# Optimization experiments

Hardware: AMD Instinct MI355X
Metric: run time of the kernel (lower is better)

## Reference

```python
import jax, jax.numpy as jnp
import numpy as np

B, S, D = 1, 4096, 2048
H, KV, HD = 16, 4, 128
ROPE_BASE = 10000.0


def setup_inputs() -> dict:
    key = jax.random.key(0)
    ks = jax.random.split(key, 5)
    hidden_states = jax.random.normal(ks[0], (B, S, D), dtype=jnp.float32) * 0.02
    Wq = jax.random.normal(ks[1], (D, H * HD), dtype=jnp.float32) * (D ** -0.5)
    Wk = jax.random.normal(ks[2], (D, KV * HD), dtype=jnp.float32) * (D ** -0.5)
    Wv = jax.random.normal(ks[3], (D, KV * HD), dtype=jnp.float32) * (D ** -0.5)
    Wo = jax.random.normal(ks[4], (H * HD, D), dtype=jnp.float32) * ((H * HD) ** -0.5)
    # causal additive mask [1,1,S,S]
    neg = jnp.float32(-1e9)
    causal = jnp.tril(jnp.ones((S, S), dtype=bool))
    attention_mask = jnp.where(causal, 0.0, neg)[None, None, :, :].astype(jnp.float32)
    position_ids = jnp.arange(S, dtype=jnp.int32)[None, :]
    return {"hidden_states": hidden_states, "Wq": Wq, "Wk": Wk, "Wv": Wv,
            "Wo": Wo, "attention_mask": attention_mask, "position_ids": position_ids}


def _rotate_half(x):
    x1, x2 = jnp.split(x, 2, axis=-1)
    return jnp.concatenate([-x2, x1], axis=-1)


def _rope_cos_sin(position_ids):
    # position_ids: [B, S] -> cos/sin [B, 1, S, HD]
    inv_freq = 1.0 / (ROPE_BASE ** (jnp.arange(0, HD, 2, dtype=jnp.float32) / HD))
    freqs = position_ids.astype(jnp.float32)[..., None] * inv_freq  # [B,S,HD/2]
    emb = jnp.concatenate([freqs, freqs], axis=-1)                   # [B,S,HD]
    return jnp.cos(emb)[:, None, :, :], jnp.sin(emb)[:, None, :, :]


def reference(hidden_states, Wq, Wk, Wv, Wo, attention_mask, position_ids):
    bsz, q_len, _ = hidden_states.shape
    # QKV projections -> [B, heads, S, HD]
    q = (hidden_states @ Wq).reshape(bsz, q_len, H, HD).transpose(0, 2, 1, 3)
    k = (hidden_states @ Wk).reshape(bsz, q_len, KV, HD).transpose(0, 2, 1, 3)
    v = (hidden_states @ Wv).reshape(bsz, q_len, KV, HD).transpose(0, 2, 1, 3)
    # inline RoPE
    cos, sin = _rope_cos_sin(position_ids)
    q = q * cos + _rotate_half(q) * sin
    k = k * cos + _rotate_half(k) * sin
    # GQA repeat_interleave on head dim
    rep = H // KV
    k = jnp.repeat(k, rep, axis=1)
    v = jnp.repeat(v, rep, axis=1)
    # attention
    scale = HD ** -0.5
    scores = jnp.einsum('bhqd,bhkd->bhqk', q, k) * scale + attention_mask
    probs = jax.nn.softmax(scores, axis=-1)
    out = jnp.einsum('bhqk,bhkd->bhqd', probs, v)
    out = out.transpose(0, 2, 1, 3).reshape(bsz, q_len, H * HD)
    return out @ Wo
```

## Files before the change

### kernel.cpp

```cpp
#include <hip/hip_runtime.h>
#include <hip/hip_bf16.h>
#include <cstdint>
#include <cmath>

#define S_LEN 4096
#define DMODEL 2048
#define NH 16
#define NKV 4
#define HD 128
#define NQKV 3072

typedef unsigned short u16;
typedef unsigned int u32;
typedef __attribute__((ext_vector_type(8))) __bf16 bf16x8;
typedef __attribute__((ext_vector_type(4))) float f32x4;
typedef __attribute__((ext_vector_type(16))) float f32x16;
typedef __attribute__((ext_vector_type(4))) int i32x4;

__device__ __forceinline__ u16 f2bf(float f) {
  __bf16 h = (__bf16)f;
  return __builtin_bit_cast(u16, h);
}
__device__ __forceinline__ float bf2f(u16 u) {
  return (float)__builtin_bit_cast(__bf16, u);
}
__device__ __forceinline__ u32 pk2(float a, float b) {
  return (u32)f2bf(a) | ((u32)f2bf(b) << 16);
}

__device__ __forceinline__ void gload16(const void* g, void* l) {
  __builtin_amdgcn_global_load_lds(
      (const __attribute__((address_space(1))) void*)g,
      (__attribute__((address_space(3))) void*)l, 16, 0, 0);
}

__global__ void k_f32_to_bf16(const float* __restrict__ src, u16* __restrict__ dst, int n4) {
  int i = blockIdx.x * blockDim.x + threadIdx.x;
  if (i < n4) {
    float4 v = reinterpret_cast<const float4*>(src)[i];
    ushort4 o = make_ushort4(f2bf(v.x), f2bf(v.y), f2bf(v.z), f2bf(v.w));
    reinterpret_cast<ushort4*>(dst)[i] = o;
  }
}

__global__ void k_transpose_f32_bf16(const float* __restrict__ src, int srcStride,
                                     u16* __restrict__ dst, int dstStride) {
  __shared__ float tile[32][33];
  int n0 = blockIdx.x * 32, k0 = blockIdx.y * 32;
  int tx = threadIdx.x, ty = threadIdx.y;
#pragma unroll
  for (int r = 0; r < 32; r += 8)
    tile[ty + r][tx] = src[(size_t)(k0 + ty + r) * srcStride + n0 + tx];
  __syncthreads();
#pragma unroll
  for (int r = 0; r < 32; r += 8)
    dst[(size_t)(n0 + ty + r) * dstStride + k0 + tx] = f2bf(tile[tx][ty + r]);
}

__global__ void k_transpose_bf16(const u16* __restrict__ src, int srcStride,
                                 u16* __restrict__ dst, int dstStride) {
  __shared__ u16 tile[32][33];
  int n0 = blockIdx.x * 32, k0 = blockIdx.y * 32;
  int tx = threadIdx.x, ty = threadIdx.y;
#pragma unroll
  for (int r = 0; r < 32; r += 8)
    tile[ty + r][tx] = src[(size_t)(k0 + ty + r) * srcStride + n0 + tx];
  __syncthreads();
#pragma unroll
  for (int r = 0; r < 32; r += 8)
    dst[(size_t)(n0 + ty + r) * dstStride + k0 + tx] = tile[tx][ty + r];
}

__global__ void k_rope_tab(const int* __restrict__ pos_ids, float2* __restrict__ tab) {
  int idx = blockIdx.x * blockDim.x + threadIdx.x;
  int s = idx >> 6, dh = idx & 63;
  const float L2B = 13.287712379549449f;
  float pos = (float)pos_ids[s];
  float invf = exp2f(-(float)dh * (L2B / 64.0f));
  float ang = pos * invf;
  tab[idx] = make_float2(cosf(ang), sinf(ang));
}

__global__ void k_rope(const u16* __restrict__ qkv, const float2* __restrict__ tab,
                       u16* __restrict__ Qb, u16* __restrict__ Kb) {
  int s = blockIdx.x;
  const u16* row = qkv + (size_t)s * NQKV;
  const float QSCALE = 0.08838834764831845f * 1.4426950408889634f;
  for (int c = threadIdx.x; c < DMODEL + NKV * HD; c += blockDim.x) {
    int d = c & 127;
    int dh = d & 63;
    float2 cs = tab[s * 64 + dh];
    float x = bf2f(row[c]);
    float xp = bf2f(row[c ^ 64]);
    float rot = (d < 64) ? -xp : xp;
    float out = x * cs.x + rot * cs.y;
    if (c < DMODEL) {
      int h = c >> 7;
      out *= QSCALE;
      Qb[((size_t)h * S_LEN + s) * HD + d] = f2bf(out);
    } else {
      int kvh = (c - DMODEL) >> 7;
      Kb[((size_t)kvh * S_LEN + s) * HD + d] = f2bf(out);
    }
  }
}

template <int OUT_BF16>
__global__ __launch_bounds__(256) void k_gemm_bt(const u16* __restrict__ A,
                                                 const u16* __restrict__ BT,
                                                 void* __restrict__ C, int M, int N, int K) {
  __shared__ __align__(16) u16 As[128 * 32];
  __shared__ __align__(16) u16 Bs[128 * 32];
  const int tid = threadIdx.x, wave = tid >> 6, lane = tid & 63;
  const int fr = lane & 15, fq = lane >> 4;
  const int rowBase = blockIdx.y * 128, colBase = blockIdx.x * 128;
  const int wr = wave >> 1, wc = wave & 1;
  f32x4 acc[4][4] = {};
  const int nk = K >> 5;
  for (int kt = 0; kt < nk; ++kt) {
    const int k0 = kt << 5;
#pragma unroll
    for (int p = 0; p < 2; ++p) {
      int cbase = p * 256 + wave * 64;
      int chunk = cbase + lane;
      int r = chunk >> 2, cb = chunk & 3;
      gload16(A + (size_t)(rowBase + r) * K + k0 + cb * 8, (char*)As + cbase * 16);
      gload16(BT + (size_t)(colBase + r) * K + k0 + cb * 8, (char*)Bs + cbase * 16);
    }
    __syncthreads();
    bf16x8 a[4], b[4];
#pragma unroll
    for (int m = 0; m < 4; ++m)
      a[m] = *reinterpret_cast<const bf16x8*>(&As[(wr * 64 + m * 16 + fr) * 32 + fq * 8]);
#pragma unroll
    for (int n = 0; n < 4; ++n)
      b[n] = *reinterpret_cast<const bf16x8*>(&Bs[(wc * 64 + n * 16 + fr) * 32 + fq * 8]);
#pragma unroll
    for (int m = 0; m < 4; ++m)
#pragma unroll
      for (int n = 0; n < 4; ++n)
        acc[m][n] = __builtin_amdgcn_mfma_f32_16x16x32_bf16(a[m], b[n], acc[m][n], 0, 0, 0);
    __syncthreads();
  }
#pragma unroll
  for (int m = 0; m < 4; ++m) {
    int row0 = rowBase + wr * 64 + m * 16 + fq * 4;
#pragma unroll
    for (int n = 0; n < 4; ++n) {
      int col = colBase + wc * 64 + n * 16 + fr;
#pragma unroll
      for (int j = 0; j < 4; ++j) {
        if (OUT_BF16)
          ((u16*)C)[(size_t)(row0 + j) * N + col] = f2bf(acc[m][n][j]);
        else
          ((float*)C)[(size_t)(row0 + j) * N + col] = acc[m][n][j];
      }
    }
  }
}

#define OP_ESTRIDE ((size_t)NH * 32 * 128 * 128)

__device__ __forceinline__ void stage_kv64(const u16* __restrict__ Kbk,
                                           const u16* __restrict__ VTk, int kb,
                                           char* KsB, char* VsB, int tid) {
#pragma unroll
  for (int it = 0; it < 2; ++it) {
    int slot = it * 512 + tid;
    int r = slot >> 4, cb = slot & 15;
    gload16(Kbk + (size_t)(kb + r) * HD + (size_t)((cb ^ (r & 15)) * 8), KsB + slot * 16);
    int vb = slot >> 7, d = slot & 127;
    gload16(VTk + (size_t)d * S_LEN + kb + vb * 8, VsB + slot * 16);
  }
}

__device__ __forceinline__ void sl_w(float* p, int off, const f32x16& v) {
#pragma unroll
  for (int r = 0; r < 16; r += 4)
    *reinterpret_cast<float4*>(p + off + r) = make_float4(v[r], v[r + 1], v[r + 2], v[r + 3]);
}

__global__ __launch_bounds__(512, 2) void k_attn(const u16* __restrict__ Qb,
                                                 const u16* __restrict__ Kb,
                                                 const u16* __restrict__ VT,
                                                 u16* __restrict__ Op,
                                                 float2* __restrict__ mlG) {
  __shared__ __align__(16) u16 Ks[2][64 * 128];
  __shared__ __align__(16) u16 Vs[2][8 * 128 * 8];
  const int h = blockIdx.x;
  const int p = blockIdx.y;
  const int e = blockIdx.z;
  const int kv = h >> 2;
  const int tid = threadIdx.x, wave = tid >> 6, lane = tid & 63;
  const int grp = wave >> 2, pr = wave & 3;
  const int ql = lane & 31, hi = lane >> 5;
  const float DEFER_THR = 11.541560327111707f;

  const u16* Kbk = Kb + (size_t)kv * S_LEN * HD;
  const u16* VTk = VT + (size_t)kv * HD * S_LEN;

#pragma unroll 1
  for (int half = 0; half < 2; ++half) {
    const int qt = half ? p : (31 - p);
    const int qg0w = qt * 128 + pr * 32;
    const int qglob = qg0w + ql;

    __syncthreads();
    stage_kv64(Kbk, VTk, e * 64, (char*)Ks[0], (char*)Vs[0], tid);

    bf16x8 qf[8];
    {
      const u16* qp = Qb + ((size_t)h * S_LEN + qglob) * HD;
#pragma unroll
      for (int t = 0; t < 8; ++t)
        qf[t] = *reinterpret_cast<const bf16x8*>(qp + t * 16 + hi * 8);
    }
    f32x16 o[4] = {};
    float m = -INFINITY, l = 0.f;

    __syncthreads();

    int buf = 0;
    const int nkt = 2 * qt + 2;
    for (int kt = e; kt < nkt; kt += 2) {
      if (kt + 2 < nkt)
        stage_kv64(Kbk, VTk, (kt + 2) * 64, (char*)Ks[buf ^ 1], (char*)Vs[buf ^ 1], tid);
      const int kbg = kt * 64 + grp * 32;
      if (kbg <= qg0w + 31) {
        const char* Kc = (const char*)Ks[buf];
        const char* Vc = (const char*)Vs[buf];

        f32x16 st = {};
        const int r0 = grp * 32 + ql;
#pragma unroll
        for (int t = 0; t < 8; ++t) {
          int ch = (2 * t + hi) ^ (ql & 15);
          bf16x8 kf = *reinterpret_cast<const bf16x8*>(Kc + r0 * 256 + ch * 16);
          st = __builtin_amdgcn_mfma_f32_32x32x16_bf16(kf, qf[t], st, 0, 0, 0);
        }
        if (kbg + 31 > qg0w) {
#pragma unroll
          for (int r = 0; r < 16; ++r) {
            int kl = (r & 3) + 8 * (r >> 2) + 4 * hi;
            if (kbg + kl > qglob) st[r] = -1e30f;
          }
        }
        float mx[16];
#pragma unroll
        for (int r = 0; r < 16; ++r) mx[r] = st[r];
#pragma unroll
        for (int s = 8; s > 0; s >>= 1)
#pragma unroll
          for (int r = 0; r < 16; ++r)
            if (r < s) mx[r] = fmaxf(mx[r], mx[r + s]);
        float tmax = fmaxf(mx[0], __shfl_xor(mx[0], 32));
        if (__any(tmax - m > DEFER_THR)) {
          float mn = fmaxf(m, tmax);
          float corr = exp2f(m - mn);
          m = mn;
          l *= corr;
#pragma unroll
          for (int d0 = 0; d0 < 4; ++d0) o[d0] *= corr;
        }
        float sm[16];
#pragma unroll
        for (int r = 0; r < 16; ++r) {
          st[r] = exp2f(st[r] - m);
          sm[r] = st[r];
        }
#pragma unroll
        for (int s = 8; s > 0; s >>= 1)
#pragma unroll
          for (int r = 0; r < 16; ++r)
            if (r < s) sm[r] += sm[r + s];
        l += sm[0] + __shfl_xor(sm[0], 32);

        bf16x8 pa0, pa1;
        {
          u32 w0 = pk2(st[0], st[1]), w1 = pk2(st[2], st[3]);
          u32 w2 = pk2(st[4], st[5]), w3 = pk2(st[6], st[7]);
          u32 xw0 = (u32)__shfl_xor((int)w0, 32), xw1 = (u32)__shfl_xor((int)w1, 32);
          u32 xw2 = (u32)__shfl_xor((int)w2, 32), xw3 = (u32)__shfl_xor((int)w3, 32);
          i32x4 pw;
          pw[0] = (int)(hi ? xw2 : w0);
          pw[1] = (int)(hi ? xw3 : w1);
          pw[2] = (int)(hi ? w2 : xw0);
          pw[3] = (int)(hi ? w3 : xw1);
          pa0 = __builtin_bit_cast(bf16x8, pw);
          w0 = pk2(st[8], st[9]);   w1 = pk2(st[10], st[11]);
          w2 = pk2(st[12], st[13]); w3 = pk2(st[14], st[15]);
          xw0 = (u32)__shfl_xor((int)w0, 32); xw1 = (u32)__shfl_xor((int)w1, 32);
          xw2 = (u32)__shfl_xor((int)w2, 32); xw3 = (u32)__shfl_xor((int)w3, 32);
          pw[0] = (int)(hi ? xw2 : w0);
          pw[1] = (int)(hi ? xw3 : w1);
          pw[2] = (int)(hi ? w2 : xw0);
          pw[3] = (int)(hi ? w3 : xw1);
          pa1 = __builtin_bit_cast(bf16x8, pw);
        }
#pragma unroll
        for (int d0 = 0; d0 < 4; ++d0) {
          int dr = d0 * 32 + ql;
          bf16x8 vf0 = *reinterpret_cast<const bf16x8*>(
              Vc + (((grp * 4 + 0 + hi) * 128) + dr) * 16);
          o[d0] = __builtin_amdgcn_mfma_f32_32x32x16_bf16(vf0, pa0, o[d0], 0, 0, 0);
          bf16x8 vf1 = *reinterpret_cast<const bf16x8*>(
              Vc + (((grp * 4 + 2 + hi) * 128) + dr) * 16);
          o[d0] = __builtin_amdgcn_mfma_f32_32x32x16_bf16(vf1, pa1, o[d0], 0, 0, 0);
        }
      }
      __syncthreads();
      buf ^= 1;
    }

    float2* mlb = (float2*)Ks;
    if (hi == 0) mlb[(grp * 4 + pr) * 32 + ql] = make_float2(m, l);
    __syncthreads();
    float2 pml = mlb[((1 - grp) * 4 + pr) * 32 + ql];
    float mm = fmaxf(m, pml.x);
    float fa = (mm > -INFINITY) ? exp2f(m - mm) : 0.f;
    float fb = (mm > -INFINITY) ? exp2f(pml.x - mm) : 0.f;
    float ll = l * fa + pml.y * fb;
    __syncthreads();
    float* exK = (float*)Ks;
    float* exV = (float*)Vs;
    const int off = (pr * 64 + lane) * 16;
    if (grp == 0) {
      sl_w(exK, off, o[2]);
      sl_w(exK + 4096, off, o[3]);
    } else {
      sl_w(exV, off, o[0]);
      sl_w(exV + 4096, off, o[1]);
    }
    if (grp == 0 && hi == 0)
      mlG[(((size_t)e * NH + h) * 32 + qt) * 128 + pr * 32 + ql] = make_float2(mm, ll);
    __syncthreads();
    {
      u16* opRow = Op + (size_t)e * OP_ESTRIDE +
                   (((size_t)h * 32 + qt) * 128 + pr * 32 + ql) * 128;
      if (grp == 0) {
#pragma unroll
        for (int rp = 0; rp < 8; ++rp) {
          int r = 2 * rp;
          int dbase = (r & 3) + 8 * (r >> 2) + 4 * hi;
          float q0a = exV[off + r], q0b = exV[off + r + 1];
          float q1a = exV[4096 + off + r], q1b = exV[4096 + off + r + 1];
          *reinterpret_cast<u32*>(opRow + 0 * 32 + dbase) =
              pk2(o[0][r] * fa + q0a * fb, o[0][r + 1] * fa + q0b * fb);
          *reinterpret_cast<u32*>(opRow + 1 * 32 + dbase) =
              pk2(o[1][r] * fa + q1a * fb, o[1][r + 1] * fa + q1b * fb);
        }
      } else {
#pragma unroll
        for (int rp = 0; rp < 8; ++rp) {
          int r = 2 * rp;
          int dbase = (r & 3) + 8 * (r >> 2) + 4 * hi;
          float q2a = exK[off + r], q2b = exK[off + r + 1];
          float q3a = exK[4096 + off + r], q3b = exK[4096 + off + r + 1];
          *reinterpret_cast<u32*>(opRow + 2 * 32 + dbase) =
              pk2(o[2][r] * fa + q2a * fb, o[2][r + 1] * fa + q2b * fb);
          *reinterpret_cast<u32*>(opRow + 3 * 32 + dbase) =
              pk2(o[3][r] * fa + q3a * fb, o[3][r + 1] * fa + q3b * fb);
        }
      }
    }
  }
}

__global__ void k_comb(const u16* __restrict__ Op, const float2* __restrict__ mlG,
                       u16* __restrict__ AO) {
  int s = blockIdx.x, h = blockIdx.y;
  int qt = s >> 7, row = s & 127;
  int t = threadIdx.x;
  size_t base = (((size_t)h * 32 + qt) * 128 + row) * 128;
  float2 ml0 = mlG[(((size_t)0 * NH + h) * 32 + qt) * 128 + row];
  float2 ml1 = mlG[(((size_t)1 * NH + h) * 32 + qt) * 128 + row];
  float M = fmaxf(ml0.x, ml1.x);
  float w0 = (ml0.x > -INFINITY) ? exp2f(ml0.x - M) : 0.f;
  float w1 = (ml1.x > -INFINITY) ? exp2f(ml1.x - M) : 0.f;
  float inv = 1.0f / (ml0.y * w0 + ml1.y * w1);
  u32 a = *reinterpret_cast<const u32*>(Op + base + t * 2);
  u32 b = *reinterpret_cast<const u32*>(Op + OP_ESTRIDE + base + t * 2);
  float o0 = bf2f((u16)a) * w0 + bf2f((u16)b) * w1;
  float o1 = bf2f((u16)(a >> 16)) * w0 + bf2f((u16)(b >> 16)) * w1;
  *reinterpret_cast<u32*>(AO + (size_t)s * DMODEL + h * HD + t * 2) = pk2(o0 * inv, o1 * inv);
}

extern "C" void kernel_launch(void* const* d_in, const int* in_sizes, int n_in,
                              void* d_out, int out_size, void* d_ws, size_t ws_size,
                              hipStream_t stream) {
  const float* hidden = (const float*)d_in[0];
  const float* Wq = (const float*)d_in[1];
  const float* Wk = (const float*)d_in[2];
  const float* Wv = (const float*)d_in[3];
  const float* Wo = (const float*)d_in[4];
  const int* pos_ids = (const int*)d_in[6];
  float* out = (float*)d_out;

  char* ws = (char*)d_ws;
  u16* WoT  = (u16*)(ws);
  u16* Wt   = (u16*)(ws + (8ull << 20));
  u16* Qb   = (u16*)(ws + (8ull << 20));
  u16* Kb   = (u16*)(ws + (24ull << 20));
  u16* VT   = (u16*)(ws + (28ull << 20));
  u16* Xb   = (u16*)(ws + (32ull << 20));
  u16* AO   = (u16*)(ws + (32ull << 20));
  float2* tab = (float2*)(ws + (48ull << 20));
  u16* QKVb = (u16*)(ws + (50ull << 20));
  u16* Op   = (u16*)(ws + (48ull << 20));
  float2* mlG = (float2*)(ws + (80ull << 20));

  dim3 tb(32, 8);
  k_f32_to_bf16<<<dim3((S_LEN * DMODEL / 4) / 256), dim3(256), 0, stream>>>(
      hidden, Xb, S_LEN * DMODEL / 4);
  k_transpose_f32_bf16<<<dim3(64, 64), tb, 0, stream>>>(Wq, 2048, Wt, 2048);
  k_transpose_f32_bf16<<<dim3(16, 64), tb, 0, stream>>>(Wk, 512, Wt + (size_t)2048 * 2048, 2048);
  k_transpose_f32_bf16<<<dim3(16, 64), tb, 0, stream>>>(Wv, 512, Wt + (size_t)2560 * 2048, 2048);
  k_transpose_f32_bf16<<<dim3(64, 64), tb, 0, stream>>>(Wo, 2048, WoT, 2048);
  k_rope_tab<<<dim3(S_LEN * 64 / 256), dim3(256), 0, stream>>>(pos_ids, tab);

  k_gemm_bt<1><<<dim3(24, 32), 256, 0, stream>>>(Xb, Wt, QKVb, S_LEN, NQKV, DMODEL);

  k_rope<<<dim3(S_LEN), 256, 0, stream>>>(QKVb, tab, Qb, Kb);
  k_transpose_bf16<<<dim3(16, 128), tb, 0, stream>>>(QKVb + 2560, NQKV, VT, S_LEN);

  k_attn<<<dim3(NH, 16, 2), 512, 0, stream>>>(Qb, Kb, VT, Op, mlG);
  k_comb<<<dim3(S_LEN, NH), 64, 0, stream>>>(Op, mlG, AO);

  k_gemm_bt<0><<<dim3(16, 32), 256, 0, stream>>>(AO, WoT, out, S_LEN, DMODEL, DMODEL);
}
```

Before: 337.7 us.

## Restructure attention into 256-thread blocks per query tile and vectorize RoPE

```diff
diff --git a/kernel.cpp b/kernel.cpp
--- a/kernel.cpp
+++ b/kernel.cpp
@@ -86,22 +86,39 @@
   int s = blockIdx.x;
   const u16* row = qkv + (size_t)s * NQKV;
   const float QSCALE = 0.08838834764831845f * 1.4426950408889634f;
-  for (int c = threadIdx.x; c < DMODEL + NKV * HD; c += blockDim.x) {
+  const int NV = (DMODEL + NKV * HD) / 8;
+  for (int v8 = threadIdx.x; v8 < NV; v8 += blockDim.x) {
+    int c = v8 * 8;
     int d = c & 127;
-    int dh = d & 63;
-    float2 cs = tab[s * 64 + dh];
-    float x = bf2f(row[c]);
-    float xp = bf2f(row[c ^ 64]);
-    float rot = (d < 64) ? -xp : xp;
-    float out = x * cs.x + rot * cs.y;
-    if (c < DMODEL) {
+    int dh0 = d & 63;
+    bool lowh = (d < 64);
+    ushort4 a0 = *reinterpret_cast<const ushort4*>(row + c);
+    ushort4 a1 = *reinterpret_cast<const ushort4*>(row + c + 4);
+    ushort4 b0 = *reinterpret_cast<const ushort4*>(row + (c ^ 64));
+    ushort4 b1 = *reinterpret_cast<const ushort4*>(row + (c ^ 64) + 4);
+    u16 xs[8] = {a0.x, a0.y, a0.z, a0.w, a1.x, a1.y, a1.z, a1.w};
+    u16 xp[8] = {b0.x, b0.y, b0.z, b0.w, b1.x, b1.y, b1.z, b1.w};
+    u16 ov[8];
+    bool isQ = (c < DMODEL);
+#pragma unroll
+    for (int e = 0; e < 8; ++e) {
+      float2 cs = tab[s * 64 + dh0 + e];
+      float x = bf2f(xs[e]);
+      float r = lowh ? -bf2f(xp[e]) : bf2f(xp[e]);
+      float o = x * cs.x + r * cs.y;
+      if (isQ) o *= QSCALE;
+      ov[e] = f2bf(o);
+    }
+    u16* dst;
+    if (isQ) {
       int h = c >> 7;
-      out *= QSCALE;
-      Qb[((size_t)h * S_LEN + s) * HD + d] = f2bf(out);
+      dst = Qb + ((size_t)h * S_LEN + s) * HD + d;
     } else {
       int kvh = (c - DMODEL) >> 7;
-      Kb[((size_t)kvh * S_LEN + s) * HD + d] = f2bf(out);
-    }
+      dst = Kb + ((size_t)kvh * S_LEN + s) * HD + d;
+    }
+    *reinterpret_cast<ushort4*>(dst) = make_ushort4(ov[0], ov[1], ov[2], ov[3]);
+    *reinterpret_cast<ushort4*>(dst + 4) = make_ushort4(ov[4], ov[5], ov[6], ov[7]);
   }
 }
 
@@ -161,12 +178,12 @@
 
 #define OP_ESTRIDE ((size_t)NH * 32 * 128 * 128)
 
-__device__ __forceinline__ void stage_kv64(const u16* __restrict__ Kbk,
+__device__ __forceinline__ void stage_kv32(const u16* __restrict__ Kbk,
                                            const u16* __restrict__ VTk, int kb,
                                            char* KsB, char* VsB, int tid) {
 #pragma unroll
   for (int it = 0; it < 2; ++it) {
-    int slot = it * 512 + tid;
+    int slot = it * 256 + tid;
     int r = slot >> 4, cb = slot & 15;
     gload16(Kbk + (size_t)(kb + r) * HD + (size_t)((cb ^ (r & 15)) * 8), KsB + slot * 16);
     int vb = slot >> 7, d = slot & 127;
@@ -174,195 +191,145 @@
   }
 }
 
-__device__ __forceinline__ void sl_w(float* p, int off, const f32x16& v) {
-#pragma unroll
-  for (int r = 0; r < 16; r += 4)
-    *reinterpret_cast<float4*>(p + off + r) = make_float4(v[r], v[r + 1], v[r + 2], v[r + 3]);
-}
-
-__global__ __launch_bounds__(512, 2) void k_attn(const u16* __restrict__ Qb,
+__global__ __launch_bounds__(256, 4) void k_attn(const u16* __restrict__ Qb,
                                                  const u16* __restrict__ Kb,
                                                  const u16* __restrict__ VT,
                                                  u16* __restrict__ Op,
                                                  float2* __restrict__ mlG) {
-  __shared__ __align__(16) u16 Ks[2][64 * 128];
-  __shared__ __align__(16) u16 Vs[2][8 * 128 * 8];
+  __shared__ __align__(16) u16 Ks[2][32 * 128];
+  __shared__ __align__(16) u16 Vs[2][4 * 128 * 8];
   const int h = blockIdx.x;
-  const int p = blockIdx.y;
+  const int qi = blockIdx.y;
   const int e = blockIdx.z;
+  const int qt = 31 - qi;
   const int kv = h >> 2;
   const int tid = threadIdx.x, wave = tid >> 6, lane = tid & 63;
-  const int grp = wave >> 2, pr = wave & 3;
   const int ql = lane & 31, hi = lane >> 5;
+  const int qg0w = qt * 128 + wave * 32;
+  const int qglob = qg0w + ql;
   const float DEFER_THR = 11.541560327111707f;
 
   const u16* Kbk = Kb + (size_t)kv * S_LEN * HD;
   const u16* VTk = VT + (size_t)kv * HD * S_LEN;
 
-#pragma unroll 1
-  for (int half = 0; half < 2; ++half) {
-    const int qt = half ? p : (31 - p);
-    const int qg0w = qt * 128 + pr * 32;
-    const int qglob = qg0w + ql;
-
+  stage_kv32(Kbk, VTk, e * 32, (char*)Ks[0], (char*)Vs[0], tid);
+
+  bf16x8 qf[8];
+  {
+    const u16* qp = Qb + ((size_t)h * S_LEN + qglob) * HD;
+#pragma unroll
+    for (int t = 0; t < 8; ++t)
+      qf[t] = *reinterpret_cast<const bf16x8*>(qp + t * 16 + hi * 8);
+  }
+  f32x16 o[4] = {};
+  float m = -INFINITY, l = 0.f;
+
+  __syncthreads();
+
+  int buf = 0;
+  const int nkt = (qt + 1) * 4;
+  for (int kt = e; kt < nkt; kt += 2) {
+    if (kt + 2 < nkt)
+      stage_kv32(Kbk, VTk, (kt + 2) * 32, (char*)Ks[buf ^ 1], (char*)Vs[buf ^ 1], tid);
+    const int kb = kt * 32;
+    if (kb <= qg0w + 31) {
+      const char* Kc = (const char*)Ks[buf];
+      const char* Vc = (const char*)Vs[buf];
+
+      f32x16 st = {};
+#pragma unroll
+      for (int t = 0; t < 8; ++t) {
+        bf16x8 kf = *reinterpret_cast<const bf16x8*>(
+            Kc + ql * 256 + (((2 * t + hi) ^ (ql & 15)) * 16));
+        st = __builtin_amdgcn_mfma_f32_32x32x16_bf16(kf, qf[t], st, 0, 0, 0);
+      }
+      if (kb + 31 > qg0w) {
+#pragma unroll
+        for (int r = 0; r < 16; ++r) {
+          int kl = (r & 3) + 8 * (r >> 2) + 4 * hi;
+          if (kb + kl > qglob) st[r] = -1e30f;
+        }
+      }
+      float mx[16];
+#pragma unroll
+      for (int r = 0; r < 16; ++r) mx[r] = st[r];
+#pragma unroll
+      for (int s = 8; s > 0; s >>= 1)
+#pragma unroll
+        for (int r = 0; r < 16; ++r)
+          if (r < s) mx[r] = fmaxf(mx[r], mx[r + s]);
+      float tmax = fmaxf(mx[0], __shfl_xor(mx[0], 32));
+      if (__any(tmax - m > DEFER_THR)) {
+        float mn = fmaxf(m, tmax);
+        float corr = exp2f(m - mn);
+        m = mn;
+        l *= corr;
+#pragma unroll
+        for (int d0 = 0; d0 < 4; ++d0) o[d0] *= corr;
+      }
+      float sm[16];
+#pragma unroll
+      for (int r = 0; r < 16; ++r) {
+        st[r] = exp2f(st[r] - m);
+        sm[r] = st[r];
+      }
+#pragma unroll
+      for (int s = 8; s > 0; s >>= 1)
+#pragma unroll
+        for (int r = 0; r < 16; ++r)
+          if (r < s) sm[r] += sm[r + s];
+      l += sm[0] + __shfl_xor(sm[0], 32);
+
+      bf16x8 pa0, pa1;
+      {
+        u32 w0 = pk2(st[0], st[1]), w1 = pk2(st[2], st[3]);
+        u32 w2 = pk2(st[4], st[5]), w3 = pk2(st[6], st[7]);
+        u32 xw0 = (u32)__shfl_xor((int)w0, 32), xw1 = (u32)__shfl_xor((int)w1, 32);
+        u32 xw2 = (u32)__shfl_xor((int)w2, 32), xw3 = (u32)__shfl_xor((int)w3, 32);
+        i32x4 pw;
+        pw[0] = (int)(hi ? xw2 : w0);
+        pw[1] = (int)(hi ? xw3 : w1);
+        pw[2] = (int)(hi ? w2 : xw0);
+        pw[3] = (int)(hi ? w3 : xw1);
+        pa0 = __builtin_bit_cast(bf16x8, pw);
+        w0 = pk2(st[8], st[9]);   w1 = pk2(st[10], st[11]);
+        w2 = pk2(st[12], st[13]); w3 = pk2(st[14], st[15]);
+        xw0 = (u32)__shfl_xor((int)w0, 32); xw1 = (u32)__shfl_xor((int)w1, 32);
+        xw2 = (u32)__shfl_xor((int)w2, 32); xw3 = (u32)__shfl_xor((int)w3, 32);
+        pw[0] = (int)(hi ? xw2 : w0);
+        pw[1] = (int)(hi ? xw3 : w1);
+        pw[2] = (int)(hi ? w2 : xw0);
+        pw[3] = (int)(hi ? w3 : xw1);
+        pa1 = __builtin_bit_cast(bf16x8, pw);
+      }
+#pragma unroll
+      for (int d0 = 0; d0 < 4; ++d0) {
+        int dr = d0 * 32 + ql;
+        bf16x8 vf0 = *reinterpret_cast<const bf16x8*>(
+            Vc + (((0 * 2 + hi) * 128) + dr) * 16);
+        o[d0] = __builtin_amdgcn_mfma_f32_32x32x16_bf16(vf0, pa0, o[d0], 0, 0, 0);
+        bf16x8 vf1 = *reinterpret_cast<const bf16x8*>(
+            Vc + (((1 * 2 + hi) * 128) + dr) * 16);
+        o[d0] = __builtin_amdgcn_mfma_f32_32x32x16_bf16(vf1, pa1, o[d0], 0, 0, 0);
+      }
+    }
     __syncthreads();
-    stage_kv64(Kbk, VTk, e * 64, (char*)Ks[0], (char*)Vs[0], tid);
-
-    bf16x8 qf[8];
-    {
-      const u16* qp = Qb + ((size_t)h * S_LEN + qglob) * HD;
-#pragma unroll
-      for (int t = 0; t < 8; ++t)
-        qf[t] = *reinterpret_cast<const bf16x8*>(qp + t * 16 + hi * 8);
-    }
-    f32x16 o[4] = {};
-    float m = -INFINITY, l = 0.f;
-
-    __syncthreads();
-
-    int buf = 0;
-    const int nkt = 2 * qt + 2;
-    for (int kt = e; kt < nkt; kt += 2) {
-      if (kt + 2 < nkt)
-        stage_kv64(Kbk, VTk, (kt + 2) * 64, (char*)Ks[buf ^ 1], (char*)Vs[buf ^ 1], tid);
-      const int kbg = kt * 64 + grp * 32;
-      if (kbg <= qg0w + 31) {
-        const char* Kc = (const char*)Ks[buf];
-        const char* Vc = (const char*)Vs[buf];
-
-        f32x16 st = {};
-        const int r0 = grp * 32 + ql;
-#pragma unroll
-        for (int t = 0; t < 8; ++t) {
-          int ch = (2 * t + hi) ^ (ql & 15);
-          bf16x8 kf = *reinterpret_cast<const bf16x8*>(Kc + r0 * 256 + ch * 16);
-          st = __builtin_amdgcn_mfma_f32_32x32x16_bf16(kf, qf[t], st, 0, 0, 0);
-        }
-        if (kbg + 31 > qg0w) {
-#pragma unroll
-          for (int r = 0; r < 16; ++r) {
-            int kl = (r & 3) + 8 * (r >> 2) + 4 * hi;
-            if (kbg + kl > qglob) st[r] = -1e30f;
-          }
-        }
-        float mx[16];
-#pragma unroll
-        for (int r = 0; r < 16; ++r) mx[r] = st[r];
-#pragma unroll
-        for (int s = 8; s > 0; s >>= 1)
-#pragma unroll
-          for (int r = 0; r < 16; ++r)
-            if (r < s) mx[r] = fmaxf(mx[r], mx[r + s]);
-        float tmax = fmaxf(mx[0], __shfl_xor(mx[0], 32));
-        if (__any(tmax - m > DEFER_THR)) {
-          float mn = fmaxf(m, tmax);
-          float corr = exp2f(m - mn);
-          m = mn;
-          l *= corr;
-#pragma unroll
-          for (int d0 = 0; d0 < 4; ++d0) o[d0] *= corr;
-        }
-        float sm[16];
-#pragma unroll
-        for (int r = 0; r < 16; ++r) {
-          st[r] = exp2f(st[r] - m);
-          sm[r] = st[r];
-        }
-#pragma unroll
-        for (int s = 8; s > 0; s >>= 1)
-#pragma unroll
-          for (int r = 0; r < 16; ++r)
-            if (r < s) sm[r] += sm[r + s];
-        l += sm[0] + __shfl_xor(sm[0], 32);
-
-        bf16x8 pa0, pa1;
-        {
-          u32 w0 = pk2(st[0], st[1]), w1 = pk2(st[2], st[3]);
-          u32 w2 = pk2(st[4], st[5]), w3 = pk2(st[6], st[7]);
-          u32 xw0 = (u32)__shfl_xor((int)w0, 32), xw1 = (u32)__shfl_xor((int)w1, 32);
-          u32 xw2 = (u32)__shfl_xor((int)w2, 32), xw3 = (u32)__shfl_xor((int)w3, 32);
-          i32x4 pw;
-          pw[0] = (int)(hi ? xw2 : w0);
-          pw[1] = (int)(hi ? xw3 : w1);
-          pw[2] = (int)(hi ? w2 : xw0);
-          pw[3] = (int)(hi ? w3 : xw1);
-          pa0 = __builtin_bit_cast(bf16x8, pw);
-          w0 = pk2(st[8], st[9]);   w1 = pk2(st[10], st[11]);
-          w2 = pk2(st[12], st[13]); w3 = pk2(st[14], st[15]);
-          xw0 = (u32)__shfl_xor((int)w0, 32); xw1 = (u32)__shfl_xor((int)w1, 32);
-          xw2 = (u32)__shfl_xor((int)w2, 32); xw3 = (u32)__shfl_xor((int)w3, 32);
-          pw[0] = (int)(hi ? xw2 : w0);
-          pw[1] = (int)(hi ? xw3 : w1);
-          pw[2] = (int)(hi ? w2 : xw0);
-          pw[3] = (int)(hi ? w3 : xw1);
-          pa1 = __builtin_bit_cast(bf16x8, pw);
-        }
-#pragma unroll
-        for (int d0 = 0; d0 < 4; ++d0) {
-          int dr = d0 * 32 + ql;
-          bf16x8 vf0 = *reinterpret_cast<const bf16x8*>(
-              Vc + (((grp * 4 + 0 + hi) * 128) + dr) * 16);
-          o[d0] = __builtin_amdgcn_mfma_f32_32x32x16_bf16(vf0, pa0, o[d0], 0, 0, 0);
-          bf16x8 vf1 = *reinterpret_cast<const bf16x8*>(
-              Vc + (((grp * 4 + 2 + hi) * 128) + dr) * 16);
-          o[d0] = __builtin_amdgcn_mfma_f32_32x32x16_bf16(vf1, pa1, o[d0], 0, 0, 0);
-        }
-      }
-      __syncthreads();
-      buf ^= 1;
-    }
-
-    float2* mlb = (float2*)Ks;
-    if (hi == 0) mlb[(grp * 4 + pr) * 32 + ql] = make_float2(m, l);
-    __syncthreads();
-    float2 pml = mlb[((1 - grp) * 4 + pr) * 32 + ql];
-    float mm = fmaxf(m, pml.x);
-    float fa = (mm > -INFINITY) ? exp2f(m - mm) : 0.f;
-    float fb = (mm > -INFINITY) ? exp2f(pml.x - mm) : 0.f;
-    float ll = l * fa + pml.y * fb;
-    __syncthreads();
-    float* exK = (float*)Ks;
-    float* exV = (float*)Vs;
-    const int off = (pr * 64 + lane) * 16;
-    if (grp == 0) {
-      sl_w(exK, off, o[2]);
-      sl_w(exK + 4096, off, o[3]);
-    } else {
-      sl_w(exV, off, o[0]);
-      sl_w(exV + 4096, off, o[1]);
-    }
-    if (grp == 0 && hi == 0)
-      mlG[(((size_t)e * NH + h) * 32 + qt) * 128 + pr * 32 + ql] = make_float2(mm, ll);
-    __syncthreads();
-    {
-      u16* opRow = Op + (size_t)e * OP_ESTRIDE +
-                   (((size_t)h * 32 + qt) * 128 + pr * 32 + ql) * 128;
-      if (grp == 0) {
-#pragma unroll
-        for (int rp = 0; rp < 8; ++rp) {
-          int r = 2 * rp;
-          int dbase = (r & 3) + 8 * (r >> 2) + 4 * hi;
-          float q0a = exV[off + r], q0b = exV[off + r + 1];
-          float q1a = exV[4096 + off + r], q1b = exV[4096 + off + r + 1];
-          *reinterpret_cast<u32*>(opRow + 0 * 32 + dbase) =
-              pk2(o[0][r] * fa + q0a * fb, o[0][r + 1] * fa + q0b * fb);
-          *reinterpret_cast<u32*>(opRow + 1 * 32 + dbase) =
-              pk2(o[1][r] * fa + q1a * fb, o[1][r + 1] * fa + q1b * fb);
-        }
-      } else {
-#pragma unroll
-        for (int rp = 0; rp < 8; ++rp) {
-          int r = 2 * rp;
-          int dbase = (r & 3) + 8 * (r >> 2) + 4 * hi;
-          float q2a = exK[off + r], q2b = exK[off + r + 1];
-          float q3a = exK[4096 + off + r], q3b = exK[4096 + off + r + 1];
-          *reinterpret_cast<u32*>(opRow + 2 * 32 + dbase) =
-              pk2(o[2][r] * fa + q2a * fb, o[2][r + 1] * fa + q2b * fb);
-          *reinterpret_cast<u32*>(opRow + 3 * 32 + dbase) =
-              pk2(o[3][r] * fa + q3a * fb, o[3][r + 1] * fa + q3b * fb);
-        }
-      }
-    }
+    buf ^= 1;
+  }
+
+  {
+    u16* opRow = Op + (size_t)e * OP_ESTRIDE +
+                 (((size_t)h * 32 + qt) * 128 + wave * 32 + ql) * 128;
+#pragma unroll
+    for (int d0 = 0; d0 < 4; ++d0)
+#pragma unroll
+      for (int rp = 0; rp < 8; ++rp) {
+        int r = 2 * rp;
+        int dbase = (r & 3) + 8 * (r >> 2) + 4 * hi;
+        *reinterpret_cast<u32*>(opRow + d0 * 32 + dbase) = pk2(o[d0][r], o[d0][r + 1]);
+      }
+    if (hi == 0)
+      mlG[(((size_t)e * NH + h) * 32 + qt) * 128 + wave * 32 + ql] = make_float2(m, l);
   }
 }
 
@@ -423,7 +390,7 @@
   k_rope<<<dim3(S_LEN), 256, 0, stream>>>(QKVb, tab, Qb, Kb);
   k_transpose_bf16<<<dim3(16, 128), tb, 0, stream>>>(QKVb + 2560, NQKV, VT, S_LEN);
 
-  k_attn<<<dim3(NH, 16, 2), 512, 0, stream>>>(Qb, Kb, VT, Op, mlG);
+  k_attn<<<dim3(NH, 32, 2), 256, 0, stream>>>(Qb, Kb, VT, Op, mlG);
   k_comb<<<dim3(S_LEN, NH), 64, 0, stream>>>(Op, mlG, AO);
 
   k_gemm_bt<0><<<dim3(16, 32), 256, 0, stream>>>(AO, WoT, out, S_LEN, DMODEL, DMODEL);
```

After: 431.5 us. +27.8%, slower.
